# Performance work log

Hardware: AMD Instinct MI355X
Metric: run time of the kernel (lower is better)

Reference implementation:

```python
import jax, jax.numpy as jnp
import numpy as np

B, CQ, CK, CV, CO = 16, 256, 256, 256, 256
H, W = 80, 80          # query spatial size (P3-like)
KH, KW = 40, 40        # key/value spatial size (P4-like)
HEADS = 4
R2 = 2 * 2             # region_size ** 2
SCALE = 1.0 / np.float32(np.sqrt(CQ))


def conv1x1(x, w, b):
    # 1x1 conv == per-pixel linear map over channels
    return jnp.einsum('bchw,oc->bohw', x, w) + b[None, :, None, None]


def setup_inputs() -> dict:
    key = jax.random.key(0)
    ks = jax.random.split(key, 10)
    s = 0.05
    return {
        'query': jax.random.normal(ks[0], (B, CQ, H, W), jnp.float32),
        'key':   jax.random.normal(ks[1], (B, CK, KH, KW), jnp.float32),
        'wq': jax.random.normal(ks[2], (CQ, CQ), jnp.float32) * s,
        'bq': jax.random.normal(ks[3], (CQ,), jnp.float32) * s,
        'wk': jax.random.normal(ks[4], (CK, CK), jnp.float32) * s,
        'bk': jax.random.normal(ks[5], (CK,), jnp.float32) * s,
        'wv': jax.random.normal(ks[6], (CV, CV), jnp.float32) * s,
        'bv': jax.random.normal(ks[7], (CV,), jnp.float32) * s,
        'wo': jax.random.normal(ks[8], (CO, CV), jnp.float32) * s,
        'bo': jax.random.normal(ks[9], (CO,), jnp.float32) * s,
    }


def reference(query, key, wq, bq, wk, bk, wv, bv, wo, bo):
    # value defaults to key in the original module
    q = conv1x1(query, wq, bq)               # [B,CQ,H,W]
    k = conv1x1(key, wk, bk)                 # [B,CK,KH,KW]
    v = conv1x1(key, wv, bv)                 # [B,CV,KH,KW]

    b, cq, h, w = q.shape
    # All R2 'patches' in the source are the SAME interpolation (no offsets),
    # so compute it once; bilinear resize matches torch align_corners=False.
    ki = jax.image.resize(k, (b, k.shape[1], h, w), method='bilinear')
    vi = jax.image.resize(v, (b, v.shape[1], h, w), method='bilinear')

    q5 = q.reshape(b, HEADS, cq // HEADS, h, w)
    k5 = ki.reshape(b, HEADS, k.shape[1] // HEADS, h, w)
    v5 = vi.reshape(b, HEADS, v.shape[1] // HEADS, h, w)

    # per-region score; identical for every region patch
    score = jnp.einsum('bhcxy,bhcxy->bhxy', q5, k5) * SCALE     # [B,h,H,W]
    scores = jnp.broadcast_to(score[:, :, None], (b, HEADS, R2, h, w))
    # NOTE: original uses nn.Softmax(dim=3) -> normalizes over the H axis
    attn = jax.nn.softmax(scores, axis=3)                       # [B,h,R2,H,W]

    # out = sum over regions of attn * v (v identical across regions)
    out = jnp.einsum('bhrxy,bhcxy->bhcxy', attn, v5)            # [B,h,C/h,H,W]
    out = out.reshape(b, -1, h, w)                              # [B,CV,H,W]
    return conv1x1(out, wo, bo)                                 # [B,CO,H,W]
```

## Files before the change

kernel.cpp:

```cpp
#include <hip/hip_runtime.h>
#include <hip/hip_bf16.h>

typedef __bf16 bf16;
typedef __attribute__((ext_vector_type(4))) float f32x4;
typedef __attribute__((ext_vector_type(8))) __bf16 bf16x8;
typedef __attribute__((ext_vector_type(4))) __bf16 bf16x4;

static __device__ __forceinline__ void gl16(const void* g, void* l) {
  __builtin_amdgcn_global_load_lds((const __attribute__((address_space(1))) void*)g,
                                   (__attribute__((address_space(3))) void*)l, 16, 0, 0);
}
static __device__ __forceinline__ bf16x8 frag(const bf16* tile, int row, int kb) {
  return *(const bf16x8*)(tile + row * 64 + ((((kb) >> 3) ^ (row & 7)) << 3));
}

__global__ void wpre(const float* __restrict__ w0, const float* __restrict__ w1,
                     const float* __restrict__ w2, const float* __restrict__ w3,
                     bf16* __restrict__ dst) {
  const float* srcs[4] = {w0, w1, w2, w3};
  const float* s = srcs[blockIdx.y];
  bf16* d = dst + (size_t)blockIdx.y * 65536;
  int base = blockIdx.x * 2048 + threadIdx.x * 8;
  f32x4 a = *(const f32x4*)(s + base);
  f32x4 b = *(const f32x4*)(s + base + 4);
  bf16x8 v = {(bf16)a[0], (bf16)a[1], (bf16)a[2], (bf16)a[3],
              (bf16)b[0], (bf16)b[1], (bf16)b[2], (bf16)b[3]};
  *(bf16x8*)(d + base) = v;
}

__global__ __launch_bounds__(256, 3)
void qscore(const float* __restrict__ query, const bf16* __restrict__ Wq,
            const float* __restrict__ bq, const bf16* __restrict__ Kpm,
            float* __restrict__ score) {
  __shared__ alignas(16) char smem[64 * 264 * 2];
  const int t = threadIdx.x;
  const int b = blockIdx.z;
  const int p0 = blockIdx.x * 64;
  const int w = t >> 6, l = t & 63;
  const int lrow = l & 15, ksel = l >> 4;
  const int pq = t & 15, cq = t >> 4;
  const float* actb = query + (size_t)b * 256 * 6400;

  auto Bt = [&](int buf) { return (bf16*)(smem + buf * 8192); };

  f32x4 Ar[4];
  auto ALOAD = [&](int kt) {
    const int k0 = kt * 64;
#pragma unroll
    for (int j = 0; j < 4; ++j)
      Ar[j] = *(const f32x4*)(actb + (size_t)(k0 + cq * 4 + j) * 6400 + p0 + pq * 4);
  };
  auto ASTORE = [&](int buf) {
    bf16* tile = Bt(buf);
#pragma unroll
    for (int e = 0; e < 4; ++e) {
      int row = pq * 4 + e;
      bf16x4 v = {(bf16)Ar[0][e], (bf16)Ar[1][e], (bf16)Ar[2][e], (bf16)Ar[3][e]};
      *(bf16x4*)(tile + row * 64 + ((((cq >> 1) ^ (row & 7)) << 3) | ((cq & 1) << 2))) = v;
    }
  };

  f32x4 acc[4][4];
#pragma unroll
  for (int i = 0; i < 4; ++i)
#pragma unroll
    for (int j = 0; j < 4; ++j) acc[i][j] = (f32x4){0.f, 0.f, 0.f, 0.f};

  auto COMPUTE = [&](int kt, int buf) {
    const int k0 = kt * 64;
    bf16x8 af[4][2];
#pragma unroll
    for (int mi = 0; mi < 4; ++mi)
#pragma unroll
      for (int kk = 0; kk < 2; ++kk)
        af[mi][kk] = *(const bf16x8*)(Wq + (size_t)(w * 64 + mi * 16 + lrow) * 256 +
                                      k0 + kk * 32 + ksel * 8);
    bf16x8 bv[4][2];
#pragma unroll
    for (int ni = 0; ni < 4; ++ni)
#pragma unroll
      for (int kk = 0; kk < 2; ++kk)
        bv[ni][kk] = frag(Bt(buf), ni * 16 + lrow, kk * 32 + ksel * 8);
#pragma unroll
    for (int kk = 0; kk < 2; ++kk)
#pragma unroll
      for (int mi = 0; mi < 4; ++mi)
#pragma unroll
        for (int ni = 0; ni < 4; ++ni)
          acc[mi][ni] = __builtin_amdgcn_mfma_f32_16x16x32_bf16(af[mi][kk], bv[ni][kk],
                                                                acc[mi][ni], 0, 0, 0);
  };

  ALOAD(0);
  ASTORE(0);
  __syncthreads();
#pragma unroll
  for (int kt = 0; kt < 4; ++kt) {
    if (kt < 3) ALOAD(kt + 1);
    COMPUTE(kt, kt & 1);
    if (kt < 3) ASTORE((kt + 1) & 1);
    __syncthreads();
  }

  __syncthreads();
  bf16* Qs = (bf16*)smem;
#pragma unroll
  for (int mi = 0; mi < 4; ++mi) {
#pragma unroll
    for (int r = 0; r < 4; ++r) {
      int o = w * 64 + mi * 16 + ksel * 4 + r;
      float bvf = bq[o];
#pragma unroll
      for (int ni = 0; ni < 4; ++ni) {
        int px = ni * 16 + lrow;
        Qs[px * 264 + o] = (bf16)(acc[mi][ni][r] + bvf);
      }
    }
  }
  __syncthreads();

  {
    int pl = t & 63, hd = t >> 6;
    int p = p0 + pl;
    int x = p / 80, y = p % 80;
    float cx = 0.5f * x - 0.25f;
    int ix = (int)floorf(cx);
    float wx1 = cx - ix;
    int x0 = ix < 0 ? 0 : ix, x1 = (ix + 1 > 39) ? 39 : ix + 1;
    float cy = 0.5f * y - 0.25f;
    int iy = (int)floorf(cy);
    float wy1 = cy - iy;
    int y0 = iy < 0 ? 0 : iy, y1 = (iy + 1 > 39) ? 39 : iy + 1;
    float w00 = (1.f - wx1) * (1.f - wy1), w01 = (1.f - wx1) * wy1;
    float w10 = wx1 * (1.f - wy1), w11 = wx1 * wy1;
    const bf16* k00 = Kpm + ((size_t)b * 1600 + x0 * 40 + y0) * 256 + hd * 64;
    const bf16* k01 = Kpm + ((size_t)b * 1600 + x0 * 40 + y1) * 256 + hd * 64;
    const bf16* k10 = Kpm + ((size_t)b * 1600 + x1 * 40 + y0) * 256 + hd * 64;
    const bf16* k11 = Kpm + ((size_t)b * 1600 + x1 * 40 + y1) * 256 + hd * 64;
    float dot = 0.f;
#pragma unroll
    for (int i = 0; i < 8; ++i) {
      bf16x8 qv = *(const bf16x8*)(Qs + pl * 264 + hd * 64 + i * 8);
      bf16x8 a = *(const bf16x8*)(k00 + i * 8);
      bf16x8 c = *(const bf16x8*)(k01 + i * 8);
      bf16x8 d = *(const bf16x8*)(k10 + i * 8);
      bf16x8 e = *(const bf16x8*)(k11 + i * 8);
#pragma unroll
      for (int j = 0; j < 8; ++j) {
        float kup = w00 * (float)a[j] + w01 * (float)c[j] + w10 * (float)d[j] + w11 * (float)e[j];
        dot += (float)qv[j] * kup;
      }
    }
    score[((size_t)b * 4 + hd) * 6400 + p] = dot * 0.0625f;
  }
}

__global__ __launch_bounds__(512, 1)
void kv_gemm(const float* __restrict__ key,
             const bf16* __restrict__ Wk, const float* __restrict__ bk, bf16* __restrict__ Kpm,
             const bf16* __restrict__ Wv, const float* __restrict__ bv, bf16* __restrict__ Vpm) {
  __shared__ alignas(16) char smem[65536];
  const int P = 1600;
  const int t = threadIdx.x;
  const int b = blockIdx.z;
  const int m0 = blockIdx.x * 128;
  const int sel = blockIdx.y >> 1;
  const int n0 = (blockIdx.y & 1) * 128;
  const bf16* W = sel ? Wv : Wk;
  const float* bias = sel ? bv : bk;
  bf16* out = sel ? Vpm : Kpm;
  const int w = t >> 6, l = t & 63;
  const int wr = w & 1, wc = w >> 1;
  const int lrow = l & 15, koff = (l >> 4) * 8;
  const int up = t & 31, uk = t >> 5;
  const float* actb = key + (size_t)b * 256 * P;

  f32x4 Ar[4];
  f32x4 acc[4][2];
#pragma unroll
  for (int i = 0; i < 4; ++i)
#pragma unroll
    for (int j = 0; j < 2; ++j) acc[i][j] = (f32x4){0.f, 0.f, 0.f, 0.f};

  auto Ab = [&](int buf) { return (bf16*)(smem + buf * 16384); };
  auto Bb = [&](int buf) { return (bf16*)(smem + 32768 + buf * 16384); };

  auto GLOADB = [&](int kt, int buf) {
    const int k0 = kt * 64;
#pragma unroll
    for (int call = 0; call < 2; ++call) {
      int idx = call * 512 + t;
      int row = idx >> 3, u = idx & 7;
      gl16(W + (size_t)(n0 + row) * 256 + k0 + ((u ^ (row & 7)) << 3), Bb(buf) + idx * 8);
    }
  };
  auto ALOAD = [&](int kt) {
    const int k0 = kt * 64;
    int ps = m0 + up * 4;
    if (ps > P - 4) ps = P - 4;
#pragma unroll
    for (int j = 0; j < 4; ++j)
      Ar[j] = *(const f32x4*)(actb + (size_t)(k0 + uk * 4 + j) * P + ps);
  };
  auto ASTORE = [&](int buf) {
#pragma unroll
    for (int j = 0; j < 4; ++j) {
      int row = up * 4 + j;
      int cs = (uk * 4) ^ ((row & 7) << 3);
      bf16x4 v = {(bf16)Ar[0][j], (bf16)Ar[1][j], (bf16)Ar[2][j], (bf16)Ar[3][j]};
      *(bf16x4*)(Ab(buf) + row * 64 + cs) = v;
    }
  };
  auto COMPUTE = [&](int buf) {
#pragma unroll
    for (int kk = 0; kk < 2; ++kk) {
      bf16x8 af[4], bvv[2];
      const int kb = kk * 32 + koff;
#pragma unroll
      for (int i = 0; i < 4; ++i) af[i] = frag(Ab(buf), wr * 64 + i * 16 + lrow, kb);
#pragma unroll
      for (int j = 0; j < 2; ++j) bvv[j] = frag(Bb(buf), wc * 32 + j * 16 + lrow, kb);
#pragma unroll
      for (int i = 0; i < 4; ++i)
#pragma unroll
        for (int j = 0; j < 2; ++j)
          acc[i][j] = __builtin_amdgcn_mfma_f32_16x16x32_bf16(af[i], bvv[j], acc[i][j], 0, 0, 0);
    }
  };

  GLOADB(0, 0);
  ALOAD(0);
  ASTORE(0);
  __syncthreads();
#pragma unroll
  for (int kt = 0; kt < 4; ++kt) {
    const int cur = kt & 1;
    if (kt < 3) { GLOADB(kt + 1, cur ^ 1); ALOAD(kt + 1); }
    __builtin_amdgcn_sched_barrier(0);
    COMPUTE(cur);
    if (kt < 3) ASTORE(cur ^ 1);
    __syncthreads();
  }

  bf16* Sc = (bf16*)smem;
#pragma unroll
  for (int mi = 0; mi < 4; ++mi) {
#pragma unroll
    for (int ni = 0; ni < 2; ++ni) {
      int ch = wc * 32 + ni * 16 + (l & 15);
      float bvf = bias[n0 + ch];
#pragma unroll
      for (int r = 0; r < 4; ++r) {
        int p = wr * 64 + mi * 16 + (l >> 4) * 4 + r;
        Sc[p * 136 + ch] = (bf16)(acc[mi][ni][r] + bvf);
      }
    }
  }
  __syncthreads();
  bf16* ob = out + (size_t)b * P * 256;
#pragma unroll
  for (int pass = 0; pass < 4; ++pass) {
    int unit = pass * 512 + t;
    int row = unit >> 4, cu = unit & 15;
    if (m0 + row < P) {
      bf16x8 v = *(const bf16x8*)(Sc + row * 136 + cu * 8);
      *(bf16x8*)(ob + (size_t)(m0 + row) * 256 + n0 + cu * 8) = v;
    }
  }
}

__global__ void smax_kernel(float* __restrict__ score) {
  __shared__ float s[6400];
  const int hd = blockIdx.x, b = blockIdx.y, t = threadIdx.x;
  float* buf = score + ((size_t)b * 4 + hd) * 6400;
  for (int i = t; i < 6400; i += 256) s[i] = buf[i];
  __syncthreads();
  if (t < 80) {
    const int y = t;
    float m = -1e30f;
    for (int x = 0; x < 80; ++x) m = fmaxf(m, s[x * 80 + y]);
    float sum = 0.f;
    for (int x = 0; x < 80; ++x) {
      float e = __expf(s[x * 80 + y] - m);
      s[x * 80 + y] = e;
      sum += e;
    }
    float inv = 4.0f / sum;
    for (int x = 0; x < 80; ++x) buf[x * 80 + y] = s[x * 80 + y] * inv;
  }
}

__global__ void outgen_kernel(const bf16* __restrict__ Vpm, const float* __restrict__ attn,
                              bf16* __restrict__ outpm) {
  __shared__ float Vx[40][256];
  __shared__ float at[4][80];
  const int x = blockIdx.x, b = blockIdx.y, t = threadIdx.x;

  float cx = 0.5f * x - 0.25f;
  int ix = (int)floorf(cx);
  float wx1 = cx - ix, wx0 = 1.f - wx1;
  int tx0 = ix < 0 ? 0 : ix, tx1 = (ix + 1 > 39) ? 39 : ix + 1;

  const bf16* r0 = Vpm + ((size_t)b * 1600 + tx0 * 40) * 256;
  const bf16* r1 = Vpm + ((size_t)b * 1600 + tx1 * 40) * 256;
  for (int ty = 0; ty < 40; ++ty)
    Vx[ty][t] = wx0 * (float)r0[ty * 256 + t] + wx1 * (float)r1[ty * 256 + t];
  for (int i = t; i < 320; i += 256) {
    int hd = i / 80, y = i % 80;
    at[hd][y] = attn[((size_t)b * 4 + hd) * 6400 + x * 80 + y];
  }
  __syncthreads();

  const int hd = t >> 6;
  bf16* ob = outpm + ((size_t)b * 6400 + x * 80) * 256;
  for (int y = 0; y < 80; ++y) {
    float cyv = 0.5f * y - 0.25f;
    int iy = (int)floorf(cyv);
    float wy1 = cyv - iy;
    int ty0 = iy < 0 ? 0 : iy, ty1 = (iy + 1 > 39) ? 39 : iy + 1;
    float v = (1.f - wy1) * Vx[ty0][t] + wy1 * Vx[ty1][t];
    ob[(size_t)y * 256 + t] = (bf16)(at[hd][y] * v);
  }
}

__global__ __launch_bounds__(512, 1)
void gemm_out(const bf16* __restrict__ act, const bf16* __restrict__ Wo,
              const float* __restrict__ bias, float* __restrict__ out) {
  __shared__ alignas(16) char smem[65536];
  const int t = threadIdx.x;
  const int b = blockIdx.z;
  const int m0 = blockIdx.x * 128;
  const int n0 = blockIdx.y * 128;
  const int w = t >> 6, l = t & 63;
  const int wr = w & 1, wc = w >> 1;
  const int lrow = l & 15, koff = (l >> 4) * 8;
  const bf16* actb = act + (size_t)b * 6400 * 256;

  f32x4 acc[4][2];
#pragma unroll
  for (int i = 0; i < 4; ++i)
#pragma unroll
    for (int j = 0; j < 2; ++j) acc[i][j] = (f32x4){0.f, 0.f, 0.f, 0.f};

  auto Ab = [&](int buf) { return (bf16*)(smem + buf * 16384); };
  auto Bb = [&](int buf) { return (bf16*)(smem + 32768 + buf * 16384); };

  auto GLOADS = [&](int kt, int buf) {
    const int k0 = kt * 64;
#pragma unroll
    for (int call = 0; call < 2; ++call) {
      int idx = call * 512 + t;
      int row = idx >> 3, u = idx & 7;
      gl16(actb + (size_t)(m0 + row) * 256 + k0 + ((u ^ (row & 7)) << 3), Ab(buf) + idx * 8);
      gl16(Wo + (size_t)(n0 + row) * 256 + k0 + ((u ^ (row & 7)) << 3), Bb(buf) + idx * 8);
    }
  };
  auto COMPUTE = [&](int buf) {
#pragma unroll
    for (int kk = 0; kk < 2; ++kk) {
      bf16x8 af[4], bvv[2];
      const int kb = kk * 32 + koff;
#pragma unroll
      for (int i = 0; i < 4; ++i) af[i] = frag(Ab(buf), wr * 64 + i * 16 + lrow, kb);
#pragma unroll
      for (int j = 0; j < 2; ++j) bvv[j] = frag(Bb(buf), wc * 32 + j * 16 + lrow, kb);
#pragma unroll
      for (int i = 0; i < 4; ++i)
#pragma unroll
        for (int j = 0; j < 2; ++j)
          acc[i][j] = __builtin_amdgcn_mfma_f32_16x16x32_bf16(af[i], bvv[j], acc[i][j], 0, 0, 0);
    }
  };

  GLOADS(0, 0);
  __syncthreads();
#pragma unroll
  for (int kt = 0; kt < 4; ++kt) {
    const int cur = kt & 1;
    if (kt < 3) GLOADS(kt + 1, cur ^ 1);
    __builtin_amdgcn_sched_barrier(0);
    COMPUTE(cur);
    __syncthreads();
  }

  float* ob = out + (size_t)b * 256 * 6400;
#pragma unroll
  for (int mi = 0; mi < 4; ++mi) {
    int pbase = m0 + wr * 64 + mi * 16 + (l >> 4) * 4;
#pragma unroll
    for (int ni = 0; ni < 2; ++ni) {
      int o_ = n0 + wc * 32 + ni * 16 + (l & 15);
      float bvf = bias[o_];
      f32x4 v = {acc[mi][ni][0] + bvf, acc[mi][ni][1] + bvf,
                 acc[mi][ni][2] + bvf, acc[mi][ni][3] + bvf};
      *(f32x4*)(ob + (size_t)o_ * 6400 + pbase) = v;
    }
  }
}

extern "C" void kernel_launch(void* const* d_in, const int* in_sizes, int n_in,
                              void* d_out, int out_size, void* d_ws, size_t ws_size,
                              hipStream_t stream) {
  const float* query = (const float*)d_in[0];
  const float* key   = (const float*)d_in[1];
  const float* wq    = (const float*)d_in[2];
  const float* bq    = (const float*)d_in[3];
  const float* wk    = (const float*)d_in[4];
  const float* bk    = (const float*)d_in[5];
  const float* wv    = (const float*)d_in[6];
  const float* bv    = (const float*)d_in[7];
  const float* wo    = (const float*)d_in[8];
  const float* bo    = (const float*)d_in[9];

  char* ws = (char*)d_ws;
  bf16*  outpm = (bf16*)(ws);
  bf16*  Kpm   = (bf16*)(ws + 52428800);
  bf16*  Vpm   = (bf16*)(ws + 65536000);
  float* score = (float*)(ws + 78643200);
  bf16*  Wb    = (bf16*)(ws + 85196800);
  bf16* wqb = Wb, *wkb = Wb + 65536, *wvb = Wb + 131072, *wob = Wb + 196608;

  wpre<<<dim3(32, 4), 256, 0, stream>>>(wq, wk, wv, wo, Wb);
  kv_gemm<<<dim3(13, 4, 16), 512, 0, stream>>>(key, wkb, bk, Kpm, wvb, bv, Vpm);
  qscore<<<dim3(100, 1, 16), 256, 0, stream>>>(query, wqb, bq, Kpm, score);
  smax_kernel<<<dim3(4, 16), 256, 0, stream>>>(score);
  outgen_kernel<<<dim3(80, 16), 256, 0, stream>>>(Vpm, score, outpm);
  gemm_out<<<dim3(50, 2, 16), 512, 0, stream>>>(outpm, wob, bo, (float*)d_out);
}
```

Baseline: 172.9 us.

## Apply output projection at key resolution before upsampling and attention weighting

Because the output projection is linear and the bilinear upsample commutes with it per head, the code now multiplies the low-resolution values by the per-head slice of Wo (uv_gemm at 40x40). A combine kernel then upsamples those projected values, weights them by attention per head, sums over heads and adds the bias. This drops the full-resolution bf16 intermediate and the 6400-row output GEMM in exchange for four times as many low-resolution GEMM outputs and scalar upsample/combine work with large per-thread register arrays. The combine kernel uses only 160 of its 256 threads, which may limit throughput.

```diff
diff --git a/kernel.cpp b/kernel.cpp
--- a/kernel.cpp
+++ b/kernel.cpp
@@ -290,110 +290,140 @@
   }
 }
 
-__global__ void outgen_kernel(const bf16* __restrict__ Vpm, const float* __restrict__ attn,
-                              bf16* __restrict__ outpm) {
-  __shared__ float Vx[40][256];
-  __shared__ float at[4][80];
-  const int x = blockIdx.x, b = blockIdx.y, t = threadIdx.x;
+__global__ __launch_bounds__(256, 4)
+void uv_gemm(const bf16* __restrict__ Vpm, const bf16* __restrict__ Wo,
+             bf16* __restrict__ Uv) {
+  __shared__ alignas(16) bf16 Vt[64 * 64];
+  const int t = threadIdx.x;
+  const int b = blockIdx.z;
+  const int hd = blockIdx.y;
+  const int q0 = blockIdx.x * 64;
+  const int w = t >> 6, l = t & 63;
+  const int lrow = l & 15, ksel = l >> 4;
+
+  const bf16* vsrc = Vpm + ((size_t)b * 1600 + q0) * 256 + hd * 64;
+#pragma unroll
+  for (int call = 0; call < 2; ++call) {
+    int idx = (w * 2 + call) * 64 + l;
+    int q = idx >> 3, u = idx & 7;
+    gl16(vsrc + (size_t)q * 256 + ((u ^ (q & 7)) << 3), Vt + idx * 8);
+  }
+  asm volatile("s_waitcnt vmcnt(0)" ::: "memory");
+  __syncthreads();
+
+  f32x4 acc[4][4];
+#pragma unroll
+  for (int i = 0; i < 4; ++i)
+#pragma unroll
+    for (int j = 0; j < 4; ++j) acc[i][j] = (f32x4){0.f, 0.f, 0.f, 0.f};
+
+#pragma unroll
+  for (int kk = 0; kk < 2; ++kk) {
+    bf16x8 af[4], bv[4];
+#pragma unroll
+    for (int mi = 0; mi < 4; ++mi)
+      af[mi] = *(const bf16x8*)(Wo + (size_t)(w * 64 + mi * 16 + lrow) * 256 +
+                                hd * 64 + kk * 32 + ksel * 8);
+#pragma unroll
+    for (int ni = 0; ni < 4; ++ni)
+      bv[ni] = frag(Vt, ni * 16 + lrow, kk * 32 + ksel * 8);
+#pragma unroll
+    for (int mi = 0; mi < 4; ++mi)
+#pragma unroll
+      for (int ni = 0; ni < 4; ++ni)
+        acc[mi][ni] = __builtin_amdgcn_mfma_f32_16x16x32_bf16(af[mi], bv[ni], acc[mi][ni], 0, 0, 0);
+  }
+
+  bf16* ob = Uv + ((size_t)(b * 4 + hd)) * 256 * 1600;
+#pragma unroll
+  for (int mi = 0; mi < 4; ++mi) {
+#pragma unroll
+    for (int ni = 0; ni < 4; ++ni) {
+#pragma unroll
+      for (int r = 0; r < 4; ++r) {
+        int o = w * 64 + mi * 16 + ksel * 4 + r;
+        int q = q0 + ni * 16 + lrow;
+        ob[(size_t)o * 1600 + q] = (bf16)acc[mi][ni][r];
+      }
+    }
+  }
+}
+
+__global__ __launch_bounds__(256, 2)
+void combine(const bf16* __restrict__ Uv, const float* __restrict__ attn,
+             const float* __restrict__ bo, float* __restrict__ out) {
+  __shared__ bf16 Us[16 * 1600];
+  const int t = threadIdx.x;
+  const int b = blockIdx.y;
+  const int o0 = blockIdx.x * 4;
+
+  const bf16* usrc = Uv + (size_t)(b * 4) * 256 * 1600;
+#pragma unroll
+  for (int i = 0; i < 13; ++i) {
+    int idx = i * 256 + t;
+    if (idx < 3200) {
+      int row = idx / 200, u = idx % 200;
+      int hd = row >> 2, oo = row & 3;
+      bf16x8 v = *(const bf16x8*)(usrc + ((size_t)hd * 256 + o0 + oo) * 1600 + u * 8);
+      *(bf16x8*)(Us + row * 1600 + u * 8) = v;
+    }
+  }
+  __syncthreads();
+  if (t >= 160) return;
+  const int x = t % 80, oh = t / 80;
 
   float cx = 0.5f * x - 0.25f;
   int ix = (int)floorf(cx);
   float wx1 = cx - ix, wx0 = 1.f - wx1;
-  int tx0 = ix < 0 ? 0 : ix, tx1 = (ix + 1 > 39) ? 39 : ix + 1;
-
-  const bf16* r0 = Vpm + ((size_t)b * 1600 + tx0 * 40) * 256;
-  const bf16* r1 = Vpm + ((size_t)b * 1600 + tx1 * 40) * 256;
-  for (int ty = 0; ty < 40; ++ty)
-    Vx[ty][t] = wx0 * (float)r0[ty * 256 + t] + wx1 * (float)r1[ty * 256 + t];
-  for (int i = t; i < 320; i += 256) {
-    int hd = i / 80, y = i % 80;
-    at[hd][y] = attn[((size_t)b * 4 + hd) * 6400 + x * 80 + y];
-  }
-  __syncthreads();
-
-  const int hd = t >> 6;
-  bf16* ob = outpm + ((size_t)b * 6400 + x * 80) * 256;
-  for (int y = 0; y < 80; ++y) {
-    float cyv = 0.5f * y - 0.25f;
-    int iy = (int)floorf(cyv);
-    float wy1 = cyv - iy;
-    int ty0 = iy < 0 ? 0 : iy, ty1 = (iy + 1 > 39) ? 39 : iy + 1;
-    float v = (1.f - wy1) * Vx[ty0][t] + wy1 * Vx[ty1][t];
-    ob[(size_t)y * 256 + t] = (bf16)(at[hd][y] * v);
-  }
-}
-
-__global__ __launch_bounds__(512, 1)
-void gemm_out(const bf16* __restrict__ act, const bf16* __restrict__ Wo,
-              const float* __restrict__ bias, float* __restrict__ out) {
-  __shared__ alignas(16) char smem[65536];
-  const int t = threadIdx.x;
-  const int b = blockIdx.z;
-  const int m0 = blockIdx.x * 128;
-  const int n0 = blockIdx.y * 128;
-  const int w = t >> 6, l = t & 63;
-  const int wr = w & 1, wc = w >> 1;
-  const int lrow = l & 15, koff = (l >> 4) * 8;
-  const bf16* actb = act + (size_t)b * 6400 * 256;
-
-  f32x4 acc[4][2];
-#pragma unroll
-  for (int i = 0; i < 4; ++i)
-#pragma unroll
-    for (int j = 0; j < 2; ++j) acc[i][j] = (f32x4){0.f, 0.f, 0.f, 0.f};
-
-  auto Ab = [&](int buf) { return (bf16*)(smem + buf * 16384); };
-  auto Bb = [&](int buf) { return (bf16*)(smem + 32768 + buf * 16384); };
-
-  auto GLOADS = [&](int kt, int buf) {
-    const int k0 = kt * 64;
-#pragma unroll
-    for (int call = 0; call < 2; ++call) {
-      int idx = call * 512 + t;
-      int row = idx >> 3, u = idx & 7;
-      gl16(actb + (size_t)(m0 + row) * 256 + k0 + ((u ^ (row & 7)) << 3), Ab(buf) + idx * 8);
-      gl16(Wo + (size_t)(n0 + row) * 256 + k0 + ((u ^ (row & 7)) << 3), Bb(buf) + idx * 8);
-    }
-  };
-  auto COMPUTE = [&](int buf) {
-#pragma unroll
-    for (int kk = 0; kk < 2; ++kk) {
-      bf16x8 af[4], bvv[2];
-      const int kb = kk * 32 + koff;
-#pragma unroll
-      for (int i = 0; i < 4; ++i) af[i] = frag(Ab(buf), wr * 64 + i * 16 + lrow, kb);
-#pragma unroll
-      for (int j = 0; j < 2; ++j) bvv[j] = frag(Bb(buf), wc * 32 + j * 16 + lrow, kb);
-#pragma unroll
-      for (int i = 0; i < 4; ++i)
-#pragma unroll
-        for (int j = 0; j < 2; ++j)
-          acc[i][j] = __builtin_amdgcn_mfma_f32_16x16x32_bf16(af[i], bvv[j], acc[i][j], 0, 0, 0);
-    }
-  };
-
-  GLOADS(0, 0);
-  __syncthreads();
-#pragma unroll
-  for (int kt = 0; kt < 4; ++kt) {
-    const int cur = kt & 1;
-    if (kt < 3) GLOADS(kt + 1, cur ^ 1);
-    __builtin_amdgcn_sched_barrier(0);
-    COMPUTE(cur);
-    __syncthreads();
-  }
-
-  float* ob = out + (size_t)b * 256 * 6400;
-#pragma unroll
-  for (int mi = 0; mi < 4; ++mi) {
-    int pbase = m0 + wr * 64 + mi * 16 + (l >> 4) * 4;
-#pragma unroll
-    for (int ni = 0; ni < 2; ++ni) {
-      int o_ = n0 + wc * 32 + ni * 16 + (l & 15);
-      float bvf = bias[o_];
-      f32x4 v = {acc[mi][ni][0] + bvf, acc[mi][ni][1] + bvf,
-                 acc[mi][ni][2] + bvf, acc[mi][ni][3] + bvf};
-      *(f32x4*)(ob + (size_t)o_ * 6400 + pbase) = v;
+  int x0 = ix < 0 ? 0 : ix, x1 = (ix + 1 > 39) ? 39 : ix + 1;
+
+  const float* attb = attn + (size_t)b * 4 * 6400 + x * 80;
+
+  for (int oo2 = 0; oo2 < 2; ++oo2) {
+    int oo = oh * 2 + oo2;
+    float acc[80];
+#pragma unroll
+    for (int y = 0; y < 80; ++y) acc[y] = 0.f;
+
+#pragma unroll
+    for (int hd = 0; hd < 4; ++hd) {
+      const bf16* r0 = Us + (hd * 4 + oo) * 1600 + x0 * 40;
+      const bf16* r1 = Us + (hd * 4 + oo) * 1600 + x1 * 40;
+      float xc[40];
+#pragma unroll
+      for (int i = 0; i < 5; ++i) {
+        bf16x8 a = *(const bf16x8*)(r0 + i * 8);
+        bf16x8 c = *(const bf16x8*)(r1 + i * 8);
+#pragma unroll
+        for (int j = 0; j < 8; ++j)
+          xc[i * 8 + j] = wx0 * (float)a[j] + wx1 * (float)c[j];
+      }
+      const float* ah = attb + hd * 6400;
+#pragma unroll
+      for (int yc = 0; yc < 80; yc += 16) {
+        f32x4 at0 = *(const f32x4*)(ah + yc);
+        f32x4 at1 = *(const f32x4*)(ah + yc + 4);
+        f32x4 at2 = *(const f32x4*)(ah + yc + 8);
+        f32x4 at3 = *(const f32x4*)(ah + yc + 12);
+        float at[16] = {at0[0], at0[1], at0[2], at0[3], at1[0], at1[1], at1[2], at1[3],
+                        at2[0], at2[1], at2[2], at2[3], at3[0], at3[1], at3[2], at3[3]};
+#pragma unroll
+        for (int yy = 0; yy < 16; ++yy) {
+          const int y = yc + yy;
+          const int iy = (y == 0) ? -1 : ((y - 1) >> 1);
+          const int lo = iy < 0 ? 0 : iy;
+          const int hi = (iy + 1 > 39) ? 39 : iy + 1;
+          float wyh = (0.5f * y - 0.25f) - iy;
+          acc[y] += at[yy] * ((1.f - wyh) * xc[lo] + wyh * xc[hi]);
+        }
+      }
+    }
+    float bias = bo[o0 + oo];
+    float* op = out + ((size_t)b * 256 + o0 + oo) * 6400 + x * 80;
+#pragma unroll
+    for (int y = 0; y < 80; y += 4) {
+      f32x4 v = {acc[y] + bias, acc[y + 1] + bias, acc[y + 2] + bias, acc[y + 3] + bias};
+      *(f32x4*)(op + y) = v;
     }
   }
 }
@@ -413,7 +443,7 @@
   const float* bo    = (const float*)d_in[9];
 
   char* ws = (char*)d_ws;
-  bf16*  outpm = (bf16*)(ws);
+  bf16*  Uv    = (bf16*)(ws);
   bf16*  Kpm   = (bf16*)(ws + 52428800);
   bf16*  Vpm   = (bf16*)(ws + 65536000);
   float* score = (float*)(ws + 78643200);
@@ -424,6 +454,6 @@
   kv_gemm<<<dim3(13, 4, 16), 512, 0, stream>>>(key, wkb, bk, Kpm, wvb, bv, Vpm);
   qscore<<<dim3(100, 1, 16), 256, 0, stream>>>(query, wqb, bq, Kpm, score);
   smax_kernel<<<dim3(4, 16), 256, 0, stream>>>(score);
-  outgen_kernel<<<dim3(80, 16), 256, 0, stream>>>(Vpm, score, outpm);
-  gemm_out<<<dim3(50, 2, 16), 512, 0, stream>>>(outpm, wob, bo, (float*)d_out);
-}
+  uv_gemm<<<dim3(25, 4, 16), 256, 0, stream>>>(Vpm, wob, Uv);
+  combine<<<dim3(64, 16), 256, 0, stream>>>(Uv, score, bo, (float*)d_out);
+}
```

Measured after the change: 604.7 us. 3.5x slower.
